# Kernel optimization log

Measured on AMD Instinct MI355X. Metric: run time of the kernel, lower is better.

The kernel has to match this reference:

```python
import jax, jax.numpy as jnp
import numpy as np

CELL = 4  # 2 ** cell_2_pow, cell_2_pow = 2
EPS = 1e-5


def conv2d(x, w, b):
    # 3x3 conv, padding 1, NCHW / OIHW
    y = jax.lax.conv_general_dilated(
        x, w, window_strides=(1, 1), padding=((1, 1), (1, 1)),
        dimension_numbers=('NCHW', 'OIHW', 'NCHW'))
    return y + b[None, :, None, None]


def setup_inputs() -> dict:
    key = jax.random.key(0)
    ks = jax.random.split(key, 4)
    B, Cc, H, W = 8, 128, 512, 512
    nh, nw = H // CELL, W // CELL  # ctrl spatial must be padded_img / cell_sz
    return dict(
        image_pipe=jax.random.normal(ks[0], (B, 6, H, W), jnp.float32),
        ctrl_pipe=jax.random.normal(ks[1], (B, Cc, nh, nw), jnp.float32),
        w1=jax.random.normal(ks[2], (50, Cc, 3, 3), jnp.float32) * 0.03,
        b1=jnp.zeros((50,), jnp.float32),
        gamma=jnp.ones((50,), jnp.float32),
        beta=jnp.zeros((50,), jnp.float32),
        mean=jnp.zeros((50,), jnp.float32),
        var=jnp.ones((50,), jnp.float32),
        w2=jax.random.normal(ks[3], (18, 50, 3, 3), jnp.float32) * 0.05,
        b2=jnp.zeros((18,), jnp.float32),
    )


def reference(image_pipe, ctrl_pipe, w1, b1, gamma, beta, mean, var, w2, b2):
    cs = CELL
    B, C6, H, W = image_pipe.shape
    # conv_condense: Conv(Cc->50) -> ReLU -> BatchNorm2d(50, inference) -> Conv(50->18)
    h = jax.nn.relu(conv2d(ctrl_pipe, w1, b1))
    scale = gamma * jax.lax.rsqrt(var + EPS)
    h = (h - mean[None, :, None, None]) * scale[None, :, None, None] + beta[None, :, None, None]
    cond = conv2d(h, w2, b2)  # [B, 18, nh, nw]
    nh, nw = cond.shape[-2], cond.shape[-1]

    padH = (-H) % cs
    padW = (-W) % cs
    rH, rW = H + padH, W + padW
    # F.pad(img, (cell, padW+cell, cell, padH+cell)): left/right then top/bottom
    img = jnp.pad(image_pipe, ((0, 0), (0, 0), (cs, padH + cs), (cs, padW + cs)))

    # 9 cell-strided shifted views; torch loop order: i over width (outer), j over height (inner)
    stack = jnp.stack(
        [img[:, :, j * cs:j * cs + rH, i * cs:i * cs + rW]
         for i in range(3) for j in range(3)], axis=-1)  # [B, 6, rH, rW, 9]
    stack = stack.reshape(B, 2, 3, rH, rW, 9)  # 2 groups of 3 channels

    # per-pixel dynamic 9-tap weights, constant within each cs x cs cell
    wts = cond.reshape(B, 2, 9, nh, nw)
    wts = jnp.repeat(jnp.repeat(wts, cs, axis=3), cs, axis=4)  # [B, 2, 9, rH, rW]

    out = jnp.einsum('bgchwk,bgkhw->bgchw', stack, wts)  # weighted neighborhood sum
    out = out.reshape(B, 6, rH, rW)[:, :, :H, :W]
    return out
```

## Files before the change

### kernel.cpp

```cpp
#include <hip/hip_runtime.h>

typedef __attribute__((ext_vector_type(8))) short short8;
typedef __attribute__((ext_vector_type(4))) float floatx4;

__device__ __forceinline__ unsigned short f2bf(float f) {
    union { float f; unsigned int u; } v; v.f = f;
    unsigned int r = (v.u + 0x7fffu + ((v.u >> 16) & 1u)) >> 16;
    return (unsigned short)r;
}

__global__ __launch_bounds__(256) void transpose_kernel(
    const float* __restrict__ ctrl, unsigned short* __restrict__ ctrlT)
{
    __shared__ unsigned short tile[64 * 66];
    const int t = threadIdx.x;
    const int x0 = blockIdx.x * 64, ci0 = blockIdx.y * 64;
    const int b = blockIdx.z >> 7, y = blockIdx.z & 127;
#pragma unroll
    for (int it = 0; it < 4; it++) {
        int ci_l = it * 16 + (t >> 4);
        int x_l = (t & 15) * 4;
        const float4 v = *(const float4*)&ctrl[(((size_t)b * 128 + ci0 + ci_l) * 128 + y) * 128 + x0 + x_l];
        tile[(x_l + 0) * 66 + ci_l] = f2bf(v.x);
        tile[(x_l + 1) * 66 + ci_l] = f2bf(v.y);
        tile[(x_l + 2) * 66 + ci_l] = f2bf(v.z);
        tile[(x_l + 3) * 66 + ci_l] = f2bf(v.w);
    }
    __syncthreads();
#pragma unroll
    for (int it = 0; it < 2; it++) {
        int x_l = it * 32 + (t >> 3);
        int ci_l = (t & 7) * 8;
        const unsigned int* p = (const unsigned int*)&tile[x_l * 66 + ci_l];
        uint4 u = make_uint4(p[0], p[1], p[2], p[3]);
        *(uint4*)&ctrlT[(((size_t)b * 128 + y) * 128 + x0 + x_l) * 128 + ci0 + ci_l] = u;
    }
}

__global__ __launch_bounds__(256) void prep_w_kernel(
    const float* __restrict__ w1, const float* __restrict__ w2,
    unsigned short* __restrict__ w1p, unsigned short* __restrict__ w2p)
{
    int i = blockIdx.x * 256 + threadIdx.x;
    if (i < 4 * 9 * 64 * 32) {
        int ci = i & 31; int t2 = i >> 5; int co = t2 & 63; int t3 = t2 >> 6;
        int tap = t3 % 9; int c4 = t3 / 9;
        float v = 0.f;
        if (co < 50) v = w1[((size_t)co * 128 + c4 * 32 + ci) * 9 + tap];
        w1p[i] = f2bf(v);
    } else {
        int j = i - 4 * 9 * 64 * 32;
        int ci = j & 31; int t2 = j >> 5; int co = t2 & 31; int t3 = t2 >> 5;
        int tap = t3 % 9; int c4 = t3 / 9;
        int cig = c4 * 32 + ci;
        float v = 0.f;
        if (co < 18 && cig < 50) v = w2[((size_t)co * 50 + cig) * 9 + tap];
        w2p[j] = f2bf(v);
    }
}

__global__ __launch_bounds__(256) void conv1_mfma(
    const unsigned short* __restrict__ xT, const unsigned short* __restrict__ w1p,
    const float* __restrict__ b1, const float* __restrict__ gamma,
    const float* __restrict__ beta, const float* __restrict__ mean,
    const float* __restrict__ var, unsigned short* __restrict__ h)
{
    __shared__ unsigned short in_s[324 * 40];
    __shared__ unsigned short w_s[9 * 64 * 40];
    const int tid = threadIdx.x;
    const int x0 = blockIdx.x * 16, y0 = blockIdx.y * 16, b = blockIdx.z;
    const int wid = tid >> 6, lane = tid & 63;
    const int ln = lane & 15, q = lane >> 4;

    floatx4 acc[4][4];
#pragma unroll
    for (int mt = 0; mt < 4; mt++)
#pragma unroll
        for (int nt = 0; nt < 4; nt++) acc[mt][nt] = (floatx4)(0.f);

    for (int c4 = 0; c4 < 4; c4++) {
        for (int i = tid; i < 1296; i += 256) {
            int p = i >> 2, g = i & 3;
            int gy = y0 + p / 18 - 1, gx = x0 + p % 18 - 1;
            uint4 v = make_uint4(0, 0, 0, 0);
            if (gy >= 0 && gy < 128 && gx >= 0 && gx < 128)
                v = *(const uint4*)&xT[(((size_t)b * 128 + gy) * 128 + gx) * 128 + c4 * 32 + g * 8];
            *(uint4*)&in_s[p * 40 + g * 8] = v;
        }
#pragma unroll
        for (int it = 0; it < 9; it++) {
            int f = it * 256 + tid;
            int g = f & 3, co = (f >> 2) & 63, tap = f >> 8;
            uint4 v = *(const uint4*)&w1p[(((size_t)c4 * 9 + tap) * 64 + co) * 32 + g * 8];
            *(uint4*)&w_s[(tap * 64 + co) * 40 + g * 8] = v;
        }
        __syncthreads();

#pragma unroll
        for (int tap = 0; tap < 9; tap++) {
            const int dy = tap / 3, dx = tap % 3;
            short8 a[4];
#pragma unroll
            for (int mt = 0; mt < 4; mt++)
                a[mt] = *(const short8*)&in_s[((wid * 4 + mt + dy) * 18 + ln + dx) * 40 + q * 8];
#pragma unroll
            for (int nt = 0; nt < 4; nt++) {
                short8 bf = *(const short8*)&w_s[(tap * 64 + nt * 16 + ln) * 40 + q * 8];
#pragma unroll
                for (int mt = 0; mt < 4; mt++)
                    acc[mt][nt] = __builtin_amdgcn_mfma_f32_16x16x32_bf16(a[mt], bf, acc[mt][nt], 0, 0, 0);
            }
        }
        __syncthreads();
    }

#pragma unroll
    for (int nt = 0; nt < 4; nt++) {
        int co = nt * 16 + ln;
        bool real = co < 50;
        float sc = 0.f, mn = 0.f, bt = 0.f, bs = 0.f;
        if (real) {
            sc = gamma[co] * rsqrtf(var[co] + 1e-5f);
            mn = mean[co]; bt = beta[co]; bs = b1[co];
        }
#pragma unroll
        for (int mt = 0; mt < 4; mt++) {
            int gy = y0 + wid * 4 + mt;
#pragma unroll
            for (int r = 0; r < 4; r++) {
                int px = q * 4 + r;
                float v = 0.f;
                if (real) {
                    float tv = fmaxf(acc[mt][nt][r] + bs, 0.f);
                    v = (tv - mn) * sc + bt;
                }
                h[(((size_t)b * 128 + gy) * 128 + x0 + px) * 64 + co] = f2bf(v);
            }
        }
    }
}

__global__ __launch_bounds__(256) void conv2_mfma(
    const unsigned short* __restrict__ hT, const unsigned short* __restrict__ w2p,
    const float* __restrict__ b2, float* __restrict__ cond)
{
    __shared__ unsigned short in_s[324 * 40];
    __shared__ unsigned short w_s[9 * 32 * 40];
    const int tid = threadIdx.x;
    const int x0 = blockIdx.x * 16, y0 = blockIdx.y * 16, b = blockIdx.z;
    const int wid = tid >> 6, lane = tid & 63;
    const int ln = lane & 15, q = lane >> 4;

    floatx4 acc[4][2];
#pragma unroll
    for (int mt = 0; mt < 4; mt++)
#pragma unroll
        for (int nt = 0; nt < 2; nt++) acc[mt][nt] = (floatx4)(0.f);

    for (int c4 = 0; c4 < 2; c4++) {
        for (int i = tid; i < 1296; i += 256) {
            int p = i >> 2, g = i & 3;
            int gy = y0 + p / 18 - 1, gx = x0 + p % 18 - 1;
            uint4 v = make_uint4(0, 0, 0, 0);
            if (gy >= 0 && gy < 128 && gx >= 0 && gx < 128)
                v = *(const uint4*)&hT[(((size_t)b * 128 + gy) * 128 + gx) * 64 + c4 * 32 + g * 8];
            *(uint4*)&in_s[p * 40 + g * 8] = v;
        }
#pragma unroll
        for (int it = 0; it < 5; it++) {
            int f = it * 256 + tid;
            if (f < 1152) {
                int g = f & 3, co = (f >> 2) & 31, tap = f >> 7;
                uint4 v = *(const uint4*)&w2p[(((size_t)c4 * 9 + tap) * 32 + co) * 32 + g * 8];
                *(uint4*)&w_s[(tap * 32 + co) * 40 + g * 8] = v;
            }
        }
        __syncthreads();

#pragma unroll
        for (int tap = 0; tap < 9; tap++) {
            const int dy = tap / 3, dx = tap % 3;
            short8 a[4];
#pragma unroll
            for (int mt = 0; mt < 4; mt++)
                a[mt] = *(const short8*)&in_s[((wid * 4 + mt + dy) * 18 + ln + dx) * 40 + q * 8];
#pragma unroll
            for (int nt = 0; nt < 2; nt++) {
                short8 bf = *(const short8*)&w_s[(tap * 32 + nt * 16 + ln) * 40 + q * 8];
#pragma unroll
                for (int mt = 0; mt < 4; mt++)
                    acc[mt][nt] = __builtin_amdgcn_mfma_f32_16x16x32_bf16(a[mt], bf, acc[mt][nt], 0, 0, 0);
            }
        }
        __syncthreads();
    }

#pragma unroll
    for (int nt = 0; nt < 2; nt++) {
        int co = nt * 16 + ln;
        if (co < 18) {
            float bs = b2[co];
#pragma unroll
            for (int mt = 0; mt < 4; mt++) {
                int gy = y0 + wid * 4 + mt;
#pragma unroll
                for (int r = 0; r < 4; r++) {
                    int px = q * 4 + r;
                    cond[(((size_t)b * 128 + gy) * 128 + x0 + px) * 18 + co] = acc[mt][nt][r] + bs;
                }
            }
        }
    }
}

__global__ __launch_bounds__(256) void apply_kernel(
    const float* __restrict__ img, const float* __restrict__ cond,
    float* __restrict__ out)
{
    const int tid = threadIdx.x;
    const int xl = tid & 63, s = tid >> 6;
    const int x4 = blockIdx.x * 64 + xl;
    const int base = blockIdx.y * 16;
    const int b = blockIdx.z >> 1, g = blockIdx.z & 1;
    const int cyb = base >> 2;

    float4 acc[3][3];
#pragma unroll
    for (int sl = 0; sl < 3; sl++)
#pragma unroll
        for (int c = 0; c < 3; c++) acc[sl][c] = make_float4(0.f, 0.f, 0.f, 0.f);

#pragma unroll
    for (int m = 0; m <= 5; m++) {
        const int r = base + s + 4 * (m - 1);
        const bool rok = (r >= 0) && (r < 512);
        float4 v[3][3];
#pragma unroll
        for (int cc = 0; cc < 3; cc++)
#pragma unroll
            for (int i = 0; i < 3; i++) {
                int xx = x4 * 4 + i * 4 - 4;
                v[cc][i] = make_float4(0.f, 0.f, 0.f, 0.f);
                if (rok && xx >= 0 && xx < 512)
                    v[cc][i] = *(const float4*)&img[(((size_t)b * 6 + g * 3 + cc) * 512 + r) * 512 + xx];
            }
#pragma unroll
        for (int j = m - 2; j <= m; j++) {
            if (j >= 0 && j < 4) {
                const int jy = m - j;
                const int slot = j % 3;
                const float* cw = &cond[(((size_t)b * 128 + cyb + j) * 128 + x4) * 18 + g * 9];
#pragma unroll
                for (int i = 0; i < 3; i++) {
                    float wv = cw[i * 3 + jy];
#pragma unroll
                    for (int cc = 0; cc < 3; cc++) {
                        acc[slot][cc].x += v[cc][i].x * wv;
                        acc[slot][cc].y += v[cc][i].y * wv;
                        acc[slot][cc].z += v[cc][i].z * wv;
                        acc[slot][cc].w += v[cc][i].w * wv;
                    }
                }
            }
        }
        const int jd = m - 2;
        if (jd >= 0 && jd < 4) {
            const int o = base + 4 * jd + s;
            const int slot = jd % 3;
#pragma unroll
            for (int cc = 0; cc < 3; cc++) {
                *(float4*)&out[(((size_t)b * 6 + g * 3 + cc) * 512 + o) * 512 + x4 * 4] = acc[slot][cc];
                acc[slot][cc] = make_float4(0.f, 0.f, 0.f, 0.f);
            }
        }
    }
}

extern "C" void kernel_launch(void* const* d_in, const int* in_sizes, int n_in,
                              void* d_out, int out_size, void* d_ws, size_t ws_size,
                              hipStream_t stream)
{
    const float* img   = (const float*)d_in[0];
    const float* ctrl  = (const float*)d_in[1];
    const float* w1    = (const float*)d_in[2];
    const float* b1    = (const float*)d_in[3];
    const float* gamma = (const float*)d_in[4];
    const float* beta  = (const float*)d_in[5];
    const float* mean  = (const float*)d_in[6];
    const float* var   = (const float*)d_in[7];
    const float* w2    = (const float*)d_in[8];
    const float* b2    = (const float*)d_in[9];
    float* out = (float*)d_out;

    char* ws = (char*)d_ws;
    unsigned short* ctrlT = (unsigned short*)ws;
    unsigned short* hbuf  = (unsigned short*)(ws + 33554432);
    float*          cond  = (float*)(ws + 50331648);
    unsigned short* w1p   = (unsigned short*)(ws + 59768832);
    unsigned short* w2p   = (unsigned short*)(ws + 59916288);

    transpose_kernel<<<dim3(2, 2, 1024), 256, 0, stream>>>(ctrl, ctrlT);
    prep_w_kernel<<<360, 256, 0, stream>>>(w1, w2, w1p, w2p);
    conv1_mfma<<<dim3(8, 8, 8), 256, 0, stream>>>(ctrlT, w1p, b1, gamma, beta, mean, var, hbuf);
    conv2_mfma<<<dim3(8, 8, 8), 256, 0, stream>>>(hbuf, w2p, b2, cond);
    apply_kernel<<<dim3(2, 32, 16), 256, 0, stream>>>(img, cond, out);
}
```

Measured before the change: 226.8 us.

## Pad cond layout to 24 and share neighbor image columns via wave shuffles

The conv2 output is re-laid out to a padded 24-float stride, with taps grouped per row so the apply kernel can fetch three weights with one float4 load. The apply kernel now loads only its own float4 column per channel and gets the left and right neighbors through cross-lane shuffles; only edge lanes issue an extra load. The next row is prefetched one step ahead (software pipelining). Cond now aliases the ctrlT workspace region, which is safe only because ctrlT is dead after conv1. The aim is to cut redundant global loads and scalar weight loads, at the cost of shuffle instructions and extra registers.

```diff
diff --git a/kernel.cpp b/kernel.cpp
--- a/kernel.cpp
+++ b/kernel.cpp
@@ -7,6 +7,15 @@
     union { float f; unsigned int u; } v; v.f = f;
     unsigned int r = (v.u + 0x7fffu + ((v.u >> 16) & 1u)) >> 16;
     return (unsigned short)r;
+}
+
+__device__ __forceinline__ float4 shfl4(float4 v, int srcLane) {
+    float4 r;
+    r.x = __shfl(v.x, srcLane, 64);
+    r.y = __shfl(v.y, srcLane, 64);
+    r.z = __shfl(v.z, srcLane, 64);
+    r.w = __shfl(v.w, srcLane, 64);
+    return r;
 }
 
 __global__ __launch_bounds__(256) void transpose_kernel(
@@ -200,13 +209,16 @@
         int co = nt * 16 + ln;
         if (co < 18) {
             float bs = b2[co];
+            int gch = co / 9, k = co % 9;
+            int iw = k / 3, jy = k % 3;
+            int pos = gch * 12 + jy * 4 + iw;
 #pragma unroll
             for (int mt = 0; mt < 4; mt++) {
                 int gy = y0 + wid * 4 + mt;
 #pragma unroll
                 for (int r = 0; r < 4; r++) {
                     int px = q * 4 + r;
-                    cond[(((size_t)b * 128 + gy) * 128 + x0 + px) * 18 + co] = acc[mt][nt][r] + bs;
+                    cond[(((size_t)b * 128 + gy) * 128 + x0 + px) * 24 + pos] = acc[mt][nt][r] + bs;
                 }
             }
         }
@@ -223,6 +235,14 @@
     const int base = blockIdx.y * 16;
     const int b = blockIdx.z >> 1, g = blockIdx.z & 1;
     const int cyb = base >> 2;
+    const int laneL = (xl + 63) & 63;
+    const int laneR = (xl + 1) & 63;
+    const bool isL = (xl == 0), isR = (xl == 63);
+
+    const float* imgc[3];
+#pragma unroll
+    for (int cc = 0; cc < 3; cc++)
+        imgc[cc] = &img[(((size_t)b * 6 + g * 3 + cc) * 512) * 512];
 
     float4 acc[3][3];
 #pragma unroll
@@ -230,48 +250,87 @@
 #pragma unroll
         for (int c = 0; c < 3; c++) acc[sl][c] = make_float4(0.f, 0.f, 0.f, 0.f);
 
+    float4 vc[3], ec[3], vn[3], en[3];
+
+    auto load_m = [&](int m, float4 vv[3], float4 ee[3]) {
+        const int r = base + s + 4 * (m - 1);
+        if (r >= 0 && r < 512) {
+            const int xo = x4 * 4;
+            const int xe = isL ? xo - 4 : xo + 4;
+            const bool eok = (isL && x4 > 0) || (isR && x4 < 127);
+#pragma unroll
+            for (int cc = 0; cc < 3; cc++) {
+                const float* rp = imgc[cc] + (size_t)r * 512;
+                vv[cc] = *(const float4*)&rp[xo];
+                ee[cc] = make_float4(0.f, 0.f, 0.f, 0.f);
+                if (eok) ee[cc] = *(const float4*)&rp[xe];
+            }
+        } else {
+#pragma unroll
+            for (int cc = 0; cc < 3; cc++) {
+                vv[cc] = make_float4(0.f, 0.f, 0.f, 0.f);
+                ee[cc] = make_float4(0.f, 0.f, 0.f, 0.f);
+            }
+        }
+    };
+
+    load_m(0, vc, ec);
+
 #pragma unroll
     for (int m = 0; m <= 5; m++) {
-        const int r = base + s + 4 * (m - 1);
-        const bool rok = (r >= 0) && (r < 512);
-        float4 v[3][3];
-#pragma unroll
-        for (int cc = 0; cc < 3; cc++)
-#pragma unroll
-            for (int i = 0; i < 3; i++) {
-                int xx = x4 * 4 + i * 4 - 4;
-                v[cc][i] = make_float4(0.f, 0.f, 0.f, 0.f);
-                if (rok && xx >= 0 && xx < 512)
-                    v[cc][i] = *(const float4*)&img[(((size_t)b * 6 + g * 3 + cc) * 512 + r) * 512 + xx];
-            }
-#pragma unroll
-        for (int j = m - 2; j <= m; j++) {
-            if (j >= 0 && j < 4) {
+        if (m < 5) load_m(m + 1, vn, en);
+
+        const int jlo = (m - 2 > 0) ? (m - 2) : 0;
+        const int jhi = (m < 3) ? m : 3;
+
+        float4 wv[3];
+#pragma unroll
+        for (int j = 0; j < 4; j++) {
+            if (j >= jlo && j <= jhi) {
                 const int jy = m - j;
+                wv[j - jlo] = *(const float4*)&cond[
+                    (((size_t)b * 128 + cyb + j) * 128 + x4) * 24 + g * 12 + jy * 4];
+            }
+        }
+
+        float4 vL[3], vR[3];
+#pragma unroll
+        for (int cc = 0; cc < 3; cc++) {
+            vL[cc] = shfl4(vc[cc], laneL);
+            vR[cc] = shfl4(vc[cc], laneR);
+            if (isL) vL[cc] = ec[cc];
+            if (isR) vR[cc] = ec[cc];
+        }
+
+#pragma unroll
+        for (int j = 0; j < 4; j++) {
+            if (j >= jlo && j <= jhi) {
                 const int slot = j % 3;
-                const float* cw = &cond[(((size_t)b * 128 + cyb + j) * 128 + x4) * 18 + g * 9];
-#pragma unroll
-                for (int i = 0; i < 3; i++) {
-                    float wv = cw[i * 3 + jy];
-#pragma unroll
-                    for (int cc = 0; cc < 3; cc++) {
-                        acc[slot][cc].x += v[cc][i].x * wv;
-                        acc[slot][cc].y += v[cc][i].y * wv;
-                        acc[slot][cc].z += v[cc][i].z * wv;
-                        acc[slot][cc].w += v[cc][i].w * wv;
-                    }
+                const float4 w = wv[j - jlo];
+#pragma unroll
+                for (int cc = 0; cc < 3; cc++) {
+                    acc[slot][cc].x += vL[cc].x * w.x + vc[cc].x * w.y + vR[cc].x * w.z;
+                    acc[slot][cc].y += vL[cc].y * w.x + vc[cc].y * w.y + vR[cc].y * w.z;
+                    acc[slot][cc].z += vL[cc].z * w.x + vc[cc].z * w.y + vR[cc].z * w.z;
+                    acc[slot][cc].w += vL[cc].w * w.x + vc[cc].w * w.y + vR[cc].w * w.z;
                 }
             }
         }
+
         const int jd = m - 2;
-        if (jd >= 0 && jd < 4) {
+        if (jd >= 0) {
             const int o = base + 4 * jd + s;
             const int slot = jd % 3;
 #pragma unroll
             for (int cc = 0; cc < 3; cc++) {
-                *(float4*)&out[(((size_t)b * 6 + g * 3 + cc) * 512 + o) * 512 + x4 * 4] = acc[slot][cc];
+                *(float4*)&out[((((size_t)b * 6 + g * 3 + cc) * 512) + o) * 512 + x4 * 4] = acc[slot][cc];
                 acc[slot][cc] = make_float4(0.f, 0.f, 0.f, 0.f);
             }
+        }
+
+        if (m < 5) {
+#pragma unroll
+            for (int cc = 0; cc < 3; cc++) { vc[cc] = vn[cc]; ec[cc] = en[cc]; }
         }
     }
 }
@@ -294,10 +353,10 @@
 
     char* ws = (char*)d_ws;
     unsigned short* ctrlT = (unsigned short*)ws;
+    float*          cond  = (float*)ws;
     unsigned short* hbuf  = (unsigned short*)(ws + 33554432);
-    float*          cond  = (float*)(ws + 50331648);
-    unsigned short* w1p   = (unsigned short*)(ws + 59768832);
-    unsigned short* w2p   = (unsigned short*)(ws + 59916288);
+    unsigned short* w1p   = (unsigned short*)(ws + 50331648);
+    unsigned short* w2p   = (unsigned short*)(ws + 50479104);
 
     transpose_kernel<<<dim3(2, 2, 1024), 256, 0, stream>>>(ctrl, ctrlT);
     prep_w_kernel<<<360, 256, 0, stream>>>(w1, w2, w1p, w2p);
```

Result: no change. 225.6 us (-0.5%).

## Repack cond weights to padded 24-wide layout and simplify apply kernel with shuffles

Applied to the files above, without the earlier changes.

conv2 now writes the per-cell 9-tap weights in a padded 24-float layout ordered by row tap, so apply_kernel can fetch each row's three weights with one float4 load. apply_kernel drops the multi-row rolling-accumulator scheme and computes one output row per thread, loading only the centre float4 per source row. Horizontal neighbours come from wavefront shuffles, with edge lanes loading an extra float4. This cuts redundant global loads and scalar weight loads, and cond now reuses the ctrlT workspace region. The cost is four times more blocks, and neighbouring vertical cells are re-read by different blocks.

```diff
diff --git a/kernel.cpp b/kernel.cpp
--- a/kernel.cpp
+++ b/kernel.cpp
@@ -7,6 +7,15 @@
     union { float f; unsigned int u; } v; v.f = f;
     unsigned int r = (v.u + 0x7fffu + ((v.u >> 16) & 1u)) >> 16;
     return (unsigned short)r;
+}
+
+__device__ __forceinline__ float4 shfl4(float4 v, int srcLane) {
+    float4 r;
+    r.x = __shfl(v.x, srcLane, 64);
+    r.y = __shfl(v.y, srcLane, 64);
+    r.z = __shfl(v.z, srcLane, 64);
+    r.w = __shfl(v.w, srcLane, 64);
+    return r;
 }
 
 __global__ __launch_bounds__(256) void transpose_kernel(
@@ -200,13 +209,16 @@
         int co = nt * 16 + ln;
         if (co < 18) {
             float bs = b2[co];
+            int gch = co / 9, k = co % 9;
+            int iw = k / 3, jy = k % 3;
+            int pos = gch * 12 + jy * 4 + iw;
 #pragma unroll
             for (int mt = 0; mt < 4; mt++) {
                 int gy = y0 + wid * 4 + mt;
 #pragma unroll
                 for (int r = 0; r < 4; r++) {
                     int px = q * 4 + r;
-                    cond[(((size_t)b * 128 + gy) * 128 + x0 + px) * 18 + co] = acc[mt][nt][r] + bs;
+                    cond[(((size_t)b * 128 + gy) * 128 + x0 + px) * 24 + pos] = acc[mt][nt][r] + bs;
                 }
             }
         }
@@ -220,60 +232,62 @@
     const int tid = threadIdx.x;
     const int xl = tid & 63, s = tid >> 6;
     const int x4 = blockIdx.x * 64 + xl;
-    const int base = blockIdx.y * 16;
+    const int o = blockIdx.y * 4 + s;
     const int b = blockIdx.z >> 1, g = blockIdx.z & 1;
-    const int cyb = base >> 2;
-
-    float4 acc[3][3];
-#pragma unroll
-    for (int sl = 0; sl < 3; sl++)
-#pragma unroll
-        for (int c = 0; c < 3; c++) acc[sl][c] = make_float4(0.f, 0.f, 0.f, 0.f);
-
-#pragma unroll
-    for (int m = 0; m <= 5; m++) {
-        const int r = base + s + 4 * (m - 1);
+    const int cy = o >> 2;
+    const int laneL = (xl + 63) & 63, laneR = (xl + 1) & 63;
+    const bool isL = (xl == 0), isR = (xl == 63);
+    const bool eok = (isL && x4 > 0) || (isR && x4 < 127);
+    const int xo = x4 * 4;
+    const int xe = isL ? xo - 4 : xo + 4;
+
+    const float* cw = &cond[(((size_t)b * 128 + cy) * 128 + x4) * 24 + g * 12];
+    float4 w[3];
+    w[0] = *(const float4*)&cw[0];
+    w[1] = *(const float4*)&cw[4];
+    w[2] = *(const float4*)&cw[8];
+
+    float4 v[3][3], e[3][3];
+#pragma unroll
+    for (int jy = 0; jy < 3; jy++) {
+        const int r = o - 4 + 4 * jy;
         const bool rok = (r >= 0) && (r < 512);
-        float4 v[3][3];
-#pragma unroll
-        for (int cc = 0; cc < 3; cc++)
-#pragma unroll
-            for (int i = 0; i < 3; i++) {
-                int xx = x4 * 4 + i * 4 - 4;
-                v[cc][i] = make_float4(0.f, 0.f, 0.f, 0.f);
-                if (rok && xx >= 0 && xx < 512)
-                    v[cc][i] = *(const float4*)&img[(((size_t)b * 6 + g * 3 + cc) * 512 + r) * 512 + xx];
-            }
-#pragma unroll
-        for (int j = m - 2; j <= m; j++) {
-            if (j >= 0 && j < 4) {
-                const int jy = m - j;
-                const int slot = j % 3;
-                const float* cw = &cond[(((size_t)b * 128 + cyb + j) * 128 + x4) * 18 + g * 9];
-#pragma unroll
-                for (int i = 0; i < 3; i++) {
-                    float wv = cw[i * 3 + jy];
-#pragma unroll
-                    for (int cc = 0; cc < 3; cc++) {
-                        acc[slot][cc].x += v[cc][i].x * wv;
-                        acc[slot][cc].y += v[cc][i].y * wv;
-                        acc[slot][cc].z += v[cc][i].z * wv;
-                        acc[slot][cc].w += v[cc][i].w * wv;
-                    }
-                }
-            }
-        }
-        const int jd = m - 2;
-        if (jd >= 0 && jd < 4) {
-            const int o = base + 4 * jd + s;
-            const int slot = jd % 3;
-#pragma unroll
-            for (int cc = 0; cc < 3; cc++) {
-                *(float4*)&out[(((size_t)b * 6 + g * 3 + cc) * 512 + o) * 512 + x4 * 4] = acc[slot][cc];
-                acc[slot][cc] = make_float4(0.f, 0.f, 0.f, 0.f);
-            }
-        }
-    }
+#pragma unroll
+        for (int cc = 0; cc < 3; cc++) {
+            v[jy][cc] = make_float4(0.f, 0.f, 0.f, 0.f);
+            e[jy][cc] = make_float4(0.f, 0.f, 0.f, 0.f);
+            if (rok) {
+                const float* rp = &img[((((size_t)b * 6 + g * 3 + cc) * 512) + r) * 512];
+                v[jy][cc] = *(const float4*)&rp[xo];
+                if (eok) e[jy][cc] = *(const float4*)&rp[xe];
+            }
+        }
+    }
+
+    float4 acc[3];
+#pragma unroll
+    for (int cc = 0; cc < 3; cc++) acc[cc] = make_float4(0.f, 0.f, 0.f, 0.f);
+
+#pragma unroll
+    for (int jy = 0; jy < 3; jy++) {
+        const float4 wj = w[jy];
+#pragma unroll
+        for (int cc = 0; cc < 3; cc++) {
+            float4 vc = v[jy][cc];
+            float4 vL = shfl4(vc, laneL);
+            float4 vR = shfl4(vc, laneR);
+            if (isL) vL = e[jy][cc];
+            if (isR) vR = e[jy][cc];
+            acc[cc].x += vL.x * wj.x + vc.x * wj.y + vR.x * wj.z;
+            acc[cc].y += vL.y * wj.x + vc.y * wj.y + vR.y * wj.z;
+            acc[cc].z += vL.z * wj.x + vc.z * wj.y + vR.z * wj.z;
+            acc[cc].w += vL.w * wj.x + vc.w * wj.y + vR.w * wj.z;
+        }
+    }
+
+#pragma unroll
+    for (int cc = 0; cc < 3; cc++)
+        *(float4*)&out[((((size_t)b * 6 + g * 3 + cc) * 512) + o) * 512 + xo] = acc[cc];
 }
 
 extern "C" void kernel_launch(void* const* d_in, const int* in_sizes, int n_in,
@@ -294,14 +308,14 @@
 
     char* ws = (char*)d_ws;
     unsigned short* ctrlT = (unsigned short*)ws;
+    float*          cond  = (float*)ws;
     unsigned short* hbuf  = (unsigned short*)(ws + 33554432);
-    float*          cond  = (float*)(ws + 50331648);
-    unsigned short* w1p   = (unsigned short*)(ws + 59768832);
-    unsigned short* w2p   = (unsigned short*)(ws + 59916288);
+    unsigned short* w1p   = (unsigned short*)(ws + 50331648);
+    unsigned short* w2p   = (unsigned short*)(ws + 50479104);
 
     transpose_kernel<<<dim3(2, 2, 1024), 256, 0, stream>>>(ctrl, ctrlT);
     prep_w_kernel<<<360, 256, 0, stream>>>(w1, w2, w1p, w2p);
     conv1_mfma<<<dim3(8, 8, 8), 256, 0, stream>>>(ctrlT, w1p, b1, gamma, beta, mean, var, hbuf);
     conv2_mfma<<<dim3(8, 8, 8), 256, 0, stream>>>(hbuf, w2p, b2, cond);
-    apply_kernel<<<dim3(2, 32, 16), 256, 0, stream>>>(img, cond, out);
-}
+    apply_kernel<<<dim3(2, 128, 16), 256, 0, stream>>>(img, cond, out);
+}
```

Result: no change. 226.7 us (-0.0%).
